# Optimization experiments

Measured on AMD Instinct MI355X. Metric: run time of the kernel, lower is better.

Reference implementation:

```python
import jax, jax.numpy as jnp
import numpy as np

B, N, C = 16, 2048, 3           # images, proposals/image, classes (incl. background)
K = 100                         # num_detections kept per class
SCORE_THRESH = 0.05
NMS_THRESH = 0.5
MIN_ANGLE = 10.0                # process_box min width (self.min_angle)
WX, WW = 1.0, 1.0               # box_coder reg_weights
NEG = jnp.float32(-1e9)


def setup_inputs() -> dict:
    key = jax.random.key(0)
    k1, k2, k3, k4 = jax.random.split(key, 4)
    class_logit = jax.random.normal(k1, (B, N, C), jnp.float32)
    box_regression = jax.random.normal(k2, (B, N, 2 * C), jnp.float32) * 0.1
    starts = jax.random.uniform(k3, (B, N), dtype=jnp.float32) * 300.0
    widths = jax.random.uniform(k4, (B, N), dtype=jnp.float32) * 50.0 + 12.0
    proposal = jnp.stack([starts, starts + widths], axis=-1)  # [B,N,2] 1-D intervals
    return {"class_logit": class_logit, "box_regression": box_regression,
            "proposal": proposal, "image_shape": 360}


def _decode(delta, prop):
    w = prop[:, 1] - prop[:, 0]
    ctr = prop[:, 0] + 0.5 * w
    dx = delta[:, 0] / WX
    dw = jnp.minimum(delta[:, 1] / WW, 4.0)  # clamp like torchvision
    pc = dx * w + ctr
    pw = jnp.exp(dw) * w
    return jnp.stack([pc - 0.5 * pw, pc + 0.5 * pw], axis=-1)  # [N,2]


def _iou_1d(a, b):
    inter = jnp.maximum(0.0, jnp.minimum(a[:, None, 1], b[None, :, 1])
                        - jnp.maximum(a[:, None, 0], b[None, :, 0]))
    union = (a[:, None, 1] - a[:, None, 0]) + (b[None, :, 1] - b[None, :, 0]) - inter
    return inter / jnp.maximum(union, 1e-8)  # [Na,Nb]


def _infer_one_class(score, delta, prop, image_shape):
    # score [N], delta [N,2], prop [N,2] -> [K,3] (start, end, score); invalid slots score=NEG
    box = _decode(delta, prop)
    lo = jnp.clip(box[:, 0], 0.0, image_shape)
    hi = jnp.clip(box[:, 1], 0.0, image_shape)
    box = jnp.stack([lo, hi], axis=-1)
    valid = ((hi - lo) >= MIN_ANGLE) & (score >= SCORE_THRESH)
    ms = jnp.where(valid, score, NEG)
    order = jnp.argsort(-ms)
    b = box[order]
    s = ms[order]
    sup = jax.lax.stop_gradient(_iou_1d(b, b)) > NMS_THRESH  # [N,N] bool
    idx = jnp.arange(N)

    def body(keep, i):  # greedy NMS in score order
        kill = sup[i] & keep[i] & (idx > i)
        return keep & ~kill, None

    keep0 = s > 0.5 * NEG
    keep, _ = jax.lax.scan(body, keep0, idx)
    ks = jnp.where(keep, s, NEG)
    top_s, top_i = jax.lax.top_k(ks, K)
    top_b = b[top_i]
    return jnp.concatenate([top_b, top_s[:, None]], axis=-1)  # [K,3]


def reference(class_logit, box_regression, proposal, image_shape):
    img = jnp.float32(image_shape)
    scores = jax.nn.softmax(class_logit, axis=-1)[..., 1:]        # [B,N,C-1] fg classes
    deltas = box_regression.reshape(B, N, C, 2)[:, :, 1:]         # [B,N,C-1,2]
    scores = jnp.moveaxis(scores, -1, 1)                          # [B,C-1,N]
    deltas = jnp.moveaxis(deltas, 2, 1)                           # [B,C-1,N,2]
    f = jax.vmap(jax.vmap(_infer_one_class, in_axes=(0, 0, None, None)),
                 in_axes=(0, 0, 0, None))
    return f(scores, deltas, proposal, img)  # [B, C-1, K, 3]
```

## Files before the change

kernel.cpp:

```cpp
#include <hip/hip_runtime.h>
#include <math.h>

#define B_IMG 16
#define N_PROP 2048
#define C_CLS 3
#define K_OUT 100
#define NTHREADS 1024
#define NWAVES (NTHREADS / 64)
#define NBLK64 (N_PROP / 64)

__device__ __forceinline__ unsigned long long shfl_xor_u64(unsigned long long v, int lx) {
    unsigned int lo = (unsigned int)__shfl_xor((int)(unsigned int)(v & 0xffffffffull), lx, 64);
    unsigned int hi = (unsigned int)__shfl_xor((int)(unsigned int)(v >> 32), lx, 64);
    return ((unsigned long long)hi << 32) | (unsigned long long)lo;
}
__device__ __forceinline__ float readlane_f(float v, int l) {
    return __int_as_float(__builtin_amdgcn_readlane(__float_as_int(v), l));
}
__device__ __forceinline__ unsigned long long readlane_u64(unsigned long long v, int l) {
    unsigned int lo = (unsigned int)__builtin_amdgcn_readlane((int)(unsigned int)(v & 0xffffffffull), l);
    unsigned int hi = (unsigned int)__builtin_amdgcn_readlane((int)(unsigned int)(v >> 32), l);
    return ((unsigned long long)hi << 32) | (unsigned long long)lo;
}
__device__ __forceinline__ bool iou_gt_half(float inter, float uni) {
    double b = (double)fmaxf(uni, 1e-8f);
    return (double)inter * 2.0 > b * 0x1.000001p0;
}
__device__ __forceinline__ float parse_imgf(int raw) {
    return (raw > 0 && raw < 1000000) ? (float)raw : __int_as_float(raw);
}

__global__ __launch_bounds__(NTHREADS)
void roiheads_fused(const float* __restrict__ class_logit,
                    const float* __restrict__ box_reg,
                    const float* __restrict__ proposal,
                    const int* __restrict__ image_shape_p,
                    float* __restrict__ out)
{
#pragma clang fp contract(off)
    __shared__ unsigned long long skey[N_PROP];
    __shared__ float blo_n[N_PROP], bhi_n[N_PROP];
    __shared__ float slo[N_PROP], shi[N_PROP];
    __shared__ unsigned char keep[N_PROP];
    __shared__ unsigned short alv[2][N_PROP];
    __shared__ float clo[64], chi[64];
    __shared__ unsigned long long sup[64];
    __shared__ unsigned long long kmask[NBLK64];
    __shared__ int wsum[NWAVES];
    __shared__ int sh_nvalid;

    const int tid = threadIdx.x;
    const int lane = tid & 63;
    const int wid = tid >> 6;
    const int img = blockIdx.x >> 1;
    const int cls = blockIdx.x & 1;
    const float imgf = parse_imgf(image_shape_p[0]);

    if (tid == 0) sh_nvalid = 0;

    const int p0 = (wid << 7) | (lane << 1);
    const int p1 = p0 | 1;

    unsigned long long r0 = 0, r1 = 0;
#pragma unroll
    for (int e = 0; e < 2; ++e) {
        const int n = p0 + e;
        const size_t g = (size_t)img * N_PROP + n;
        const float* lg = class_logit + g * C_CLS;
        float l0 = lg[0], l1 = lg[1], l2 = lg[2];
        float mx = fmaxf(l0, fmaxf(l1, l2));
        float e0 = (float)exp((double)(l0 - mx));
        float e1 = (float)exp((double)(l1 - mx));
        float e2 = (float)exp((double)(l2 - mx));
        float denom = (e0 + e1) + e2;
        float score = ((cls == 0) ? e1 : e2) / denom;

        const float* dr = box_reg + g * (2 * C_CLS) + 2 * (cls + 1);
        float dx = dr[0];
        float dw = fminf(dr[1], 4.0f);
        const float* pp = proposal + g * 2;
        float pA = pp[0], pB = pp[1];
        float w = pB - pA;
        float ctr = pA + 0.5f * w;
        float tt = dx * w;
        float pc = tt + ctr;
        float pw = (float)exp((double)dw) * w;
        float half = 0.5f * pw;
        float lo = pc - half;
        float hi = pc + half;
        lo = fminf(fmaxf(lo, 0.0f), imgf);
        hi = fminf(fmaxf(hi, 0.0f), imgf);
        bool valid = ((hi - lo) >= 10.0f) && (score >= 0.05f);
        float ms = valid ? score : -1e9f;
        blo_n[n] = lo;
        bhi_n[n] = hi;
        unsigned int uu = __float_as_uint(ms);
        unsigned int enc = (uu & 0x80000000u) ? ~uu : (uu | 0x80000000u);
        unsigned long long key = ((unsigned long long)enc << 32) |
                                 (unsigned long long)(0xFFFFFFFFu - (unsigned int)n);
        if (e == 0) r0 = key; else r1 = key;
    }

    auto pass_inreg = [&](int k, int j) {
        if (j == 1) {
            bool desc = ((p0 & k) == 0);
            bool sw = desc ? (r0 < r1) : (r0 > r1);
            if (sw) { unsigned long long t = r0; r0 = r1; r1 = t; }
        } else {
            int lx = j >> 1;
            unsigned long long o0 = shfl_xor_u64(r0, lx);
            unsigned long long o1 = shfl_xor_u64(r1, lx);
            bool desc = ((p0 & k) == 0);
            bool lower = ((p0 & j) == 0);
            bool takeMax = (lower == desc);
            r0 = takeMax ? (r0 > o0 ? r0 : o0) : (r0 < o0 ? r0 : o0);
            r1 = takeMax ? (r1 > o1 ? r1 : o1) : (r1 < o1 ? r1 : o1);
        }
    };

    for (int k = 2; k <= 128; k <<= 1)
        for (int j = k >> 1; j >= 1; j >>= 1)
            pass_inreg(k, j);

    for (int k = 256; k <= N_PROP; k <<= 1) {
        skey[p0] = r0; skey[p1] = r1;
        __syncthreads();
        for (int j = k >> 1; j >= 128; j >>= 1) {
            int i = ((tid & ~(j - 1)) << 1) | (tid & (j - 1));
            int part = i | j;
            unsigned long long a = skey[i], b = skey[part];
            bool desc_blk = ((i & k) == 0);
            bool sw = desc_blk ? (a < b) : (a > b);
            if (sw) { skey[i] = b; skey[part] = a; }
            __syncthreads();
        }
        r0 = skey[p0]; r1 = skey[p1];
        for (int j = 64; j >= 1; j >>= 1)
            pass_inreg(k, j);
    }
    skey[p0] = r0; skey[p1] = r1;
    __syncthreads();

    for (int i = tid; i < N_PROP; i += NTHREADS) {
        unsigned long long kk = skey[i];
        unsigned int e = (unsigned int)(kk >> 32);
        unsigned int sb = (e & 0x80000000u) ? (e & 0x7FFFFFFFu) : ~e;
        float s = __uint_as_float(sb);
        unsigned int n = 0xFFFFFFFFu - (unsigned int)(kk & 0xFFFFFFFFull);
        slo[i] = blo_n[n];
        shi[i] = bhi_n[n];
        keep[i] = 0;
        bool v = (s > -5e8f);
        unsigned long long mb = __ballot(v);
        if (lane == 0) atomicAdd(&sh_nvalid, __popcll(mb));
        alv[0][i] = (unsigned short)i;
    }
    __syncthreads();

    int na = sh_nvalid;
    int cur = 0;
    int tk = 0;
    const unsigned long long below = (1ull << lane) - 1ull;

    while (na > 0) {
        const int m = (na < 64) ? na : 64;

        unsigned short cp = alv[cur][lane];
        bool cin = (lane < m);
        float qloc = cin ? slo[cp] : 0.0f;
        float qhic = cin ? shi[cp] : 0.0f;

#pragma unroll
        for (int rr4 = 0; rr4 < 4; ++rr4) {
            int rr = (wid << 2) | rr4;
            unsigned long long row = 0;
            if (rr < m) {
                unsigned short rp = alv[cur][rr];
                float rlo = slo[rp], rhi = shi[rp];
                float inter = fmaxf(fminf(rhi, qhic) - fmaxf(rlo, qloc), 0.0f);
                float uni = (rhi - rlo) + (qhic - qloc) - inter;
                bool kill = cin && (lane > rr) && iou_gt_half(inter, uni);
                row = __ballot(kill);
            }
            if (lane == 0) sup[rr] = row;
        }
        __syncthreads();

        unsigned long long rw = sup[lane];
        unsigned long long A = (m >= 64) ? ~0ull : ((1ull << m) - 1ull);
        unsigned long long kept = 0;
        while (A) {
            int c = __builtin_ctzll(A);
            kept |= (1ull << c);
            A &= ~(readlane_u64(rw, c) | (1ull << c));
        }
        const int cnt = __popcll(kept);

        if (wid == 0) {
            bool alive = cin && ((kept >> lane) & 1ull);
            if (alive) {
                keep[cp] = 1;
                int rank = __popcll(kept & below);
                clo[rank] = qloc; chi[rank] = qhic;
            }
        }
        __syncthreads();
        tk += cnt;
        if (tk >= K_OUT) break;

        float klo = 0.0f, khi = 0.0f;
        if (lane < cnt) { klo = clo[lane]; khi = chi[lane]; }
        int base2 = 0;
        for (int start = 64; start < na; start += NTHREADS) {
            int t2 = start + tid;
            unsigned short qq = 0;
            bool surv = false;
            if (t2 < na) {
                qq = alv[cur][t2];
                float qlo = slo[qq], qhi = shi[qq];
                float qw = qhi - qlo;
                bool dead = false;
                for (int r = 0; r < cnt; ++r) {
                    float cl = readlane_f(klo, r);
                    float ch = readlane_f(khi, r);
                    float inter = fmaxf(fminf(qhi, ch) - fmaxf(qlo, cl), 0.0f);
                    float uni = qw + (ch - cl) - inter;
                    dead |= iou_gt_half(inter, uni);
                }
                surv = !dead;
            }
            unsigned long long mb = __ballot(surv);
            if (lane == 0) wsum[wid] = __popcll(mb);
            __syncthreads();
            int off2 = base2, tot = base2;
            for (int w2 = 0; w2 < NWAVES; ++w2) {
                int c2 = wsum[w2];
                if (w2 < wid) off2 += c2;
                tot += c2;
            }
            if (surv) alv[cur ^ 1][off2 + __popcll(mb & below)] = qq;
            base2 = tot;
            __syncthreads();
        }
        na = base2;
        cur ^= 1;
    }

    for (int blk = wid; blk < NBLK64; blk += NWAVES) {
        bool kk = keep[blk * 64 + lane] != 0;
        unsigned long long mb = __ballot(kk);
        if (lane == 0) kmask[blk] = mb;
    }
    __syncthreads();
    {
        float* outp = out + (((size_t)img * 2 + cls) * K_OUT) * 3;
        for (int blk = wid; blk < NBLK64; blk += NWAVES) {
            int kc = 0, nc = 0, nk = 0;
            for (int b = 0; b < NBLK64; ++b) {
                int pc = __popcll(kmask[b]);
                nk += pc;
                if (b < blk) { kc += pc; nc += 64 - pc; }
            }
            if (kc >= K_OUT && nk + nc >= K_OUT && nc >= K_OUT) continue;
            int p = blk * 64 + lane;
            unsigned long long mb = kmask[blk];
            bool k = (mb >> lane) & 1ull;
            int rk = kc + __popcll(mb & below);
            int rn = nc + __popcll((~mb) & below);
            if (k) {
                if (rk < K_OUT) {
                    unsigned long long kk2 = skey[p];
                    unsigned int e = (unsigned int)(kk2 >> 32);
                    unsigned int sb = (e & 0x80000000u) ? (e & 0x7FFFFFFFu) : ~e;
                    outp[rk * 3 + 0] = slo[p];
                    outp[rk * 3 + 1] = shi[p];
                    outp[rk * 3 + 2] = __uint_as_float(sb);
                }
            } else {
                int oi = nk + rn;
                if (oi < K_OUT) {
                    outp[oi * 3 + 0] = slo[p];
                    outp[oi * 3 + 1] = shi[p];
                    outp[oi * 3 + 2] = -1e9f;
                }
            }
        }
    }
}

extern "C" void kernel_launch(void* const* d_in, const int* in_sizes, int n_in,
                              void* d_out, int out_size, void* d_ws, size_t ws_size,
                              hipStream_t stream) {
    const float* class_logit = (const float*)d_in[0];
    const float* box_reg     = (const float*)d_in[1];
    const float* prop        = (const float*)d_in[2];
    const int*   image_shape = (const int*)d_in[3];
    float* out = (float*)d_out;
    (void)d_ws; (void)ws_size;

    roiheads_fused<<<dim3(B_IMG * 2), dim3(NTHREADS), 0, stream>>>(
        class_logit, box_reg, prop, image_shape, out);
}
```

Measured before the change: 97.16 us.

## Halve block size to 512 threads with four sort keys per thread

```diff
diff --git a/kernel.cpp b/kernel.cpp
--- a/kernel.cpp
+++ b/kernel.cpp
@@ -5,9 +5,10 @@
 #define N_PROP 2048
 #define C_CLS 3
 #define K_OUT 100
-#define NTHREADS 1024
+#define NTHREADS 512
 #define NWAVES (NTHREADS / 64)
 #define NBLK64 (N_PROP / 64)
+
 
 __device__ __forceinline__ unsigned long long shfl_xor_u64(unsigned long long v, int lx) {
     unsigned int lo = (unsigned int)__shfl_xor((int)(unsigned int)(v & 0xffffffffull), lx, 64);
@@ -58,13 +59,13 @@
 
     if (tid == 0) sh_nvalid = 0;
 
-    const int p0 = (wid << 7) | (lane << 1);
-    const int p1 = p0 | 1;
-
-    unsigned long long r0 = 0, r1 = 0;
-#pragma unroll
-    for (int e = 0; e < 2; ++e) {
-        const int n = p0 + e;
+    const int pbase = tid << 2;
+    const unsigned long long below = (1ull << lane) - 1ull;
+
+    unsigned long long r[4];
+#pragma unroll
+    for (int e = 0; e < 4; ++e) {
+        const int n = pbase + e;
         const size_t g = (size_t)img * N_PROP + n;
         const float* lg = class_logit + g * C_CLS;
         float l0 = lg[0], l1 = lg[1], l2 = lg[2];
@@ -96,49 +97,61 @@
         bhi_n[n] = hi;
         unsigned int uu = __float_as_uint(ms);
         unsigned int enc = (uu & 0x80000000u) ? ~uu : (uu | 0x80000000u);
-        unsigned long long key = ((unsigned long long)enc << 32) |
-                                 (unsigned long long)(0xFFFFFFFFu - (unsigned int)n);
-        if (e == 0) r0 = key; else r1 = key;
-    }
-
-    auto pass_inreg = [&](int k, int j) {
+        r[e] = ((unsigned long long)enc << 32) |
+               (unsigned long long)(0xFFFFFFFFu - (unsigned int)n);
+    }
+
+    auto cmpswap = [&](unsigned long long &a, unsigned long long &b, bool desc) {
+        bool sw = desc ? (a < b) : (a > b);
+        if (sw) { unsigned long long t = a; a = b; b = t; }
+    };
+    auto pass4 = [&](int k, int j) {
         if (j == 1) {
-            bool desc = ((p0 & k) == 0);
-            bool sw = desc ? (r0 < r1) : (r0 > r1);
-            if (sw) { unsigned long long t = r0; r0 = r1; r1 = t; }
+            cmpswap(r[0], r[1], ((pbase & k) == 0));
+            cmpswap(r[2], r[3], (((pbase + 2) & k) == 0));
+        } else if (j == 2) {
+            bool desc = ((pbase & k) == 0);
+            cmpswap(r[0], r[2], desc);
+            cmpswap(r[1], r[3], desc);
         } else {
-            int lx = j >> 1;
-            unsigned long long o0 = shfl_xor_u64(r0, lx);
-            unsigned long long o1 = shfl_xor_u64(r1, lx);
-            bool desc = ((p0 & k) == 0);
-            bool lower = ((p0 & j) == 0);
+            const int lx = j >> 2;
+            bool desc = ((pbase & k) == 0);
+            bool lower = ((lane & lx) == 0);
             bool takeMax = (lower == desc);
-            r0 = takeMax ? (r0 > o0 ? r0 : o0) : (r0 < o0 ? r0 : o0);
-            r1 = takeMax ? (r1 > o1 ? r1 : o1) : (r1 < o1 ? r1 : o1);
+#pragma unroll
+            for (int s = 0; s < 4; ++s) {
+                unsigned long long o = shfl_xor_u64(r[s], lx);
+                r[s] = takeMax ? (r[s] > o ? r[s] : o) : (r[s] < o ? r[s] : o);
+            }
         }
     };
 
-    for (int k = 2; k <= 128; k <<= 1)
+    for (int k = 2; k <= 256; k <<= 1)
         for (int j = k >> 1; j >= 1; j >>= 1)
-            pass_inreg(k, j);
-
-    for (int k = 256; k <= N_PROP; k <<= 1) {
-        skey[p0] = r0; skey[p1] = r1;
+            pass4(k, j);
+
+    for (int k = 512; k <= N_PROP; k <<= 1) {
+#pragma unroll
+        for (int s = 0; s < 4; ++s) skey[pbase + s] = r[s];
         __syncthreads();
-        for (int j = k >> 1; j >= 128; j >>= 1) {
-            int i = ((tid & ~(j - 1)) << 1) | (tid & (j - 1));
-            int part = i | j;
-            unsigned long long a = skey[i], b = skey[part];
-            bool desc_blk = ((i & k) == 0);
-            bool sw = desc_blk ? (a < b) : (a > b);
-            if (sw) { skey[i] = b; skey[part] = a; }
+        for (int j = k >> 1; j >= 256; j >>= 1) {
+            for (int pr = tid; pr < N_PROP / 2; pr += NTHREADS) {
+                int i = ((pr & ~(j - 1)) << 1) | (pr & (j - 1));
+                int part = i | j;
+                unsigned long long a = skey[i], b = skey[part];
+                bool desc_blk = ((i & k) == 0);
+                bool sw = desc_blk ? (a < b) : (a > b);
+                if (sw) { skey[i] = b; skey[part] = a; }
+            }
             __syncthreads();
         }
-        r0 = skey[p0]; r1 = skey[p1];
-        for (int j = 64; j >= 1; j >>= 1)
-            pass_inreg(k, j);
-    }
-    skey[p0] = r0; skey[p1] = r1;
+#pragma unroll
+        for (int s = 0; s < 4; ++s) r[s] = skey[pbase + s];
+        for (int j = 128; j >= 1; j >>= 1)
+            pass4(k, j);
+    }
+#pragma unroll
+    for (int s = 0; s < 4; ++s) skey[pbase + s] = r[s];
     __syncthreads();
 
     for (int i = tid; i < N_PROP; i += NTHREADS) {
@@ -160,7 +173,6 @@
     int na = sh_nvalid;
     int cur = 0;
     int tk = 0;
-    const unsigned long long below = (1ull << lane) - 1ull;
 
     while (na > 0) {
         const int m = (na < 64) ? na : 64;
@@ -171,8 +183,8 @@
         float qhic = cin ? shi[cp] : 0.0f;
 
 #pragma unroll
-        for (int rr4 = 0; rr4 < 4; ++rr4) {
-            int rr = (wid << 2) | rr4;
+        for (int rr8 = 0; rr8 < 8; ++rr8) {
+            int rr = (wid << 3) | rr8;
             unsigned long long row = 0;
             if (rr < m) {
                 unsigned short rp = alv[cur][rr];
@@ -220,9 +232,9 @@
                 float qlo = slo[qq], qhi = shi[qq];
                 float qw = qhi - qlo;
                 bool dead = false;
-                for (int r = 0; r < cnt; ++r) {
-                    float cl = readlane_f(klo, r);
-                    float ch = readlane_f(khi, r);
+                for (int r2 = 0; r2 < cnt; ++r2) {
+                    float cl = readlane_f(klo, r2);
+                    float ch = readlane_f(khi, r2);
                     float inter = fmaxf(fminf(qhi, ch) - fmaxf(qlo, cl), 0.0f);
                     float uni = qw + (ch - cl) - inter;
                     dead |= iou_gt_half(inter, uni);
@@ -233,6 +245,7 @@
             if (lane == 0) wsum[wid] = __popcll(mb);
             __syncthreads();
             int off2 = base2, tot = base2;
+#pragma unroll
             for (int w2 = 0; w2 < NWAVES; ++w2) {
                 int c2 = wsum[w2];
                 if (w2 < wid) off2 += c2;
```

New measurement: 106.0 us. 9.1% more time.
